# Optimization experiments

Measured on AMD Instinct MI355X. Metric: run time of the kernel, lower is better.

## Reference

```python
import jax, jax.numpy as jnp
import numpy as np

C = 1024
R = 4            # reduction
A = 10           # num_adapters
LN_EPS = 1e-5
THRESHOLDS = np.array([1/9, 1/7, 1/5, 1/3, 1.0, 3.0, 5.0, 7.0, 9.0], dtype=np.float32)


def setup_inputs() -> dict:
    key = jax.random.key(0)
    k_feat, k_ar, k_w1, k_w2 = jax.random.split(key, 4)
    B, NA, H, W = 2, 3, 64, 64
    Cr = C // R
    output_feat = jax.random.normal(k_feat, (B, C, H, W), jnp.float32)
    # aspect ratios in [0,10) so all 10 adapters get selected
    aspect_ratio = jax.random.uniform(k_ar, (B, NA, H, W), jnp.float32) * 10.0
    # LayerNorm params (torch default init: weight=1, bias=0), stacked over adapters
    ln_scale = jnp.ones((A, C), jnp.float32)
    ln_bias = jnp.zeros((A, C), jnp.float32)
    # kaiming_normal_ fan_out / relu: std = sqrt(2/fan_out); torch weight [out,in]
    # w1 here is [C, Cr] == torch weight [Cr, C].T, fan_out = Cr
    w1 = jax.random.normal(k_w1, (A, C, Cr), jnp.float32) * np.sqrt(2.0 / Cr)
    # w2 here is [Cr, C] == torch weight [C, Cr].T, fan_out = C
    w2 = jax.random.normal(k_w2, (A, Cr, C), jnp.float32) * np.sqrt(2.0 / C)
    return dict(output_feat=output_feat, aspect_ratio=aspect_ratio,
                ln_scale=ln_scale, ln_bias=ln_bias, w1=w1, w2=w2)


def reference(output_feat, aspect_ratio, ln_scale, ln_bias, w1, w2):
    B, Cc, H, W = output_feat.shape
    NA = aspect_ratio.shape[1]
    HW = H * W
    # tokens [N, C]
    x = output_feat.transpose(0, 2, 3, 1).reshape(-1, Cc)
    # shared LayerNorm normalization (per-adapter affine applied after)
    mu = jnp.mean(x, axis=-1, keepdims=True)
    var = jnp.var(x, axis=-1, keepdims=True)
    norm = (x - mu) * jax.lax.rsqrt(var + LN_EPS)              # [N, C]
    y = norm[None, :, :] * ln_scale[:, None, :] + ln_bias[:, None, :]  # [A, N, C]
    h = jax.nn.gelu(jnp.einsum('anc,acd->and', y, w1), approximate=False)
    adapter_out = jnp.einsum('and,adc->anc', h, w2)            # [A, N, C]
    adapter_out = adapter_out.reshape(A, B, HW, Cc)            # [A, B, HW, C]
    # per-anchor, per-pixel adapter index from aspect ratio vs thresholds
    thr = jnp.asarray(THRESHOLDS, dtype=aspect_ratio.dtype)
    ar = aspect_ratio.reshape(B, NA, HW)
    idx = jnp.sum(ar[..., None] > thr, axis=-1)                # [B, NA, HW] in [0, 9]
    # gather selected adapter output per (batch, anchor, pixel)
    b_idx = jnp.arange(B)[:, None, None]
    p_idx = jnp.arange(HW)[None, None, :]
    selected = adapter_out[idx, b_idx, p_idx]                  # [B, NA, HW, C]
    selected = selected.mean(axis=1).reshape(B, H, W, Cc).transpose(0, 3, 1, 2)
    return selected + output_feat
```

## Files before the change

### kernel.cpp

```cpp
#include <hip/hip_runtime.h>
#include <hip/hip_bf16.h>
#include <math.h>

#define C_DIM 1024
#define CR    256
#define A_N   10
#define NANCH 3
#define B_N   2
#define HW_N  4096
#define NTOK  (B_N*HW_N)
#define KG2   (A_N*CR)

typedef unsigned short ushort_t;
typedef __attribute__((ext_vector_type(4))) float f32x4;
typedef __attribute__((ext_vector_type(8))) short bf16x8;

__device__ __forceinline__ ushort_t f2bf(float x) {
    __hip_bfloat16 h = __float2bfloat16(x);
    return *reinterpret_cast<ushort_t*>(&h);
}
__device__ __forceinline__ float bf2f(ushort_t u) {
    return __uint_as_float(((unsigned)u) << 16);
}

__device__ __forceinline__ float fast_gelu(float x) {
    float t = x * x;
    float u = x * (-1.5957691216f - 0.0713548163f * t);
    float e = __expf(u);
    return x * __frcp_rn(1.0f + e);
}

__global__ __launch_bounds__(256) void prep_all(
    const float* __restrict__ w1, const float* __restrict__ w2,
    const float* __restrict__ ln_s, const float* __restrict__ ln_b,
    const float* __restrict__ feat, const float* __restrict__ ar,
    ushort_t* __restrict__ w1t, ushort_t* __restrict__ w2t,
    float* __restrict__ bias1, float* __restrict__ sumv, float* __restrict__ sumq,
    int* __restrict__ cnt, int* __restrict__ tokw, int* __restrict__ tokmap) {
    __shared__ float lds[64][65];
    __shared__ float bb[4][64];
    __shared__ int lcnt[A_N], lpos[A_N], gbase[A_N];
    int id = blockIdx.x, tid = threadIdx.x;
    int lo = tid & 63, hi = tid >> 6;

    if (id < 640) {
        int d0 = (id & 3) * 64, c0 = ((id >> 2) & 15) * 64, a = id >> 6;
        #pragma unroll
        for (int i = 0; i < 16; i++) {
            int c_l = i * 4 + hi;
            lds[c_l][lo] = w1[((size_t)a * C_DIM + c0 + c_l) * CR + d0 + lo];
        }
        __syncthreads();
        {
            float s = 0.f;
            #pragma unroll
            for (int cc = 0; cc < 16; cc++) {
                int c = hi * 16 + cc;
                s += lds[c][lo] * ln_b[a * C_DIM + c0 + c];
            }
            bb[hi][lo] = s;
        }
        float sc = ln_s[a * C_DIM + c0 + lo];
        #pragma unroll
        for (int i = 0; i < 16; i++) {
            int d_l = i * 4 + hi;
            w1t[((size_t)a * CR + d0 + d_l) * C_DIM + c0 + lo] = f2bf(lds[lo][d_l] * sc);
        }
        __syncthreads();
        if (hi == 0)
            atomicAdd(&bias1[a * CR + d0 + lo], bb[0][lo] + bb[1][lo] + bb[2][lo] + bb[3][lo]);
    } else if (id < 1280) {
        int id2 = id - 640;
        int k0 = (id2 % 40) * 64, c0 = (id2 / 40) * 64;
        #pragma unroll
        for (int i = 0; i < 16; i++) {
            int k_l = i * 4 + hi;
            lds[k_l][lo] = w2[((size_t)k0 + k_l) * C_DIM + c0 + lo];
        }
        __syncthreads();
        #pragma unroll
        for (int i = 0; i < 16; i++) {
            int c_l = i * 4 + hi;
            w2t[((size_t)c0 + c_l) * KG2 + k0 + lo] = f2bf(lds[lo][c_l]);
        }
    } else if (id < 2304) {
        int id2 = id - 1280;
        int p0 = (id2 & 63) * 64, c0 = ((id2 >> 6) & 7) * 128, b = id2 >> 9;
        int p = lo, cs = hi;
        float s = 0.f, s2 = 0.f;
        #pragma unroll
        for (int c = cs; c < 128; c += 4) {
            float v = feat[((size_t)b * C_DIM + c0 + c) * HW_N + p0 + p];
            s += v; s2 += v * v;
        }
        float (*sh)[64] = (float(*)[64])lds;
        sh[cs][p] = s; sh[cs + 4][p] = s2;
        __syncthreads();
        if (tid < 64) {
            float ss = sh[0][tid] + sh[1][tid] + sh[2][tid] + sh[3][tid];
            float qq = sh[4][tid] + sh[5][tid] + sh[6][tid] + sh[7][tid];
            int t = b * HW_N + p0 + tid;
            atomicAdd(&sumv[t], ss);
            atomicAdd(&sumq[t], qq);
        }
    } else {
        if (tid < A_N) { lcnt[tid] = 0; lpos[tid] = 0; }
        __syncthreads();
        int t = (id - 2304) * 256 + tid;
        int b = t >> 12, p = t & (HW_N - 1);
        const float THR[9] = {1.0f/9.0f, 1.0f/7.0f, 0.2f, 1.0f/3.0f, 1.0f, 3.0f, 5.0f, 7.0f, 9.0f};
        int idxs[NANCH];
        #pragma unroll
        for (int na = 0; na < NANCH; na++) {
            float v = ar[(size_t)b * NANCH * HW_N + na * HW_N + p];
            int idx = 0;
            #pragma unroll
            for (int i = 0; i < 9; i++) idx += (v > THR[i]) ? 1 : 0;
            idxs[na] = idx;
        }
        int myA[NANCH], myC[NANCH], nmine = 0;
        #pragma unroll
        for (int j = 0; j < NANCH; j++) {
            bool first = true; int c3 = 0;
            #pragma unroll
            for (int k = 0; k < NANCH; k++) {
                if (idxs[k] == idxs[j]) { c3++; if (k < j) first = false; }
            }
            if (first) {
                myA[nmine] = idxs[j];
                myC[nmine] = c3;
                nmine++;
                atomicAdd(&lcnt[idxs[j]], 1);
            }
        }
        __syncthreads();
        if (tid < A_N) gbase[tid] = atomicAdd(&cnt[tid], lcnt[tid]);
        __syncthreads();
        for (int i = 0; i < NANCH; i++) {
            if (i < nmine) {
                int a2 = myA[i];
                int slot = atomicAdd(&lpos[a2], 1);
                int pos = gbase[a2] + slot;
                tokw[a2 * NTOK + pos] = t;
                tokmap[t * 3 + i] = pos | (a2 << 13) | (myC[i] << 17);
            } else {
                tokmap[t * 3 + i] = 0;
            }
        }
    }
}

__global__ __launch_bounds__(256) void normk(const float* __restrict__ feat,
                                             const float* __restrict__ sumv,
                                             const float* __restrict__ sumq,
                                             ushort_t* __restrict__ normG) {
    int p0 = blockIdx.x * 64, c0 = blockIdx.y * 64, b = blockIdx.z;
    __shared__ float lds[64][65];
    int tid = threadIdx.x, lo = tid & 63, hi = tid >> 6;
    #pragma unroll
    for (int i = 0; i < 16; i++) {
        int c_l = i * 4 + hi;
        lds[c_l][lo] = feat[((size_t)b * C_DIM + c0 + c_l) * HW_N + p0 + lo];
    }
    __syncthreads();
    #pragma unroll
    for (int i = 0; i < 16; i++) {
        int p_l = i * 4 + hi;
        int t = b * HW_N + p0 + p_l;
        float m = sumv[t] * (1.f / C_DIM);
        float q = sumq[t] * (1.f / C_DIM);
        float r = rsqrtf(q - m * m + 1e-5f);
        normG[(size_t)t * C_DIM + c0 + lo] = f2bf((lds[lo][p_l] - m) * r);
    }
}

__device__ __forceinline__ void gemm_core_ptrs(
    const ushort_t* const ap[4], const ushort_t* const bp[4],
    int K, ushort_t* As, ushort_t* Bs, f32x4 acc[4][4]) {
    const int tid = threadIdx.x;
    const int lane = tid & 63;
    const int w = tid >> 6;
    const int wr = w >> 1, wc = w & 1;
    const int lrow = lane & 15;
    const int quad = lane >> 4;
    const int swzr = lrow & 7;

    #pragma unroll
    for (int i = 0; i < 4; i++)
        #pragma unroll
        for (int j = 0; j < 4; j++)
            #pragma unroll
            for (int e = 0; e < 4; e++) acc[i][j][e] = 0.f;

    for (int k0 = 0; k0 < K; k0 += 64) {
        __syncthreads();
        #pragma unroll
        for (int i = 0; i < 4; i++) {
            __builtin_amdgcn_global_load_lds(
                (__attribute__((address_space(1))) void*)(ap[i] + k0),
                (__attribute__((address_space(3))) void*)(As + (w * 32 + i * 8) * 64),
                16, 0, 0);
            __builtin_amdgcn_global_load_lds(
                (__attribute__((address_space(1))) void*)(bp[i] + k0),
                (__attribute__((address_space(3))) void*)(Bs + (w * 32 + i * 8) * 64),
                16, 0, 0);
        }
        __syncthreads();
        #pragma unroll
        for (int ks = 0; ks < 2; ks++) {
            const int cidx = ((ks * 4 + quad) ^ swzr) * 8;
            bf16x8 af[4], bfr[4];
            #pragma unroll
            for (int mt = 0; mt < 4; mt++)
                af[mt] = *(const bf16x8*)(As + (wr * 64 + mt * 16 + lrow) * 64 + cidx);
            #pragma unroll
            for (int nt = 0; nt < 4; nt++)
                bfr[nt] = *(const bf16x8*)(Bs + (wc * 64 + nt * 16 + lrow) * 64 + cidx);
            #pragma unroll
            for (int mt = 0; mt < 4; mt++)
                #pragma unroll
                for (int nt = 0; nt < 4; nt++)
                    acc[mt][nt] = __builtin_amdgcn_mfma_f32_16x16x32_bf16(af[mt], bfr[nt], acc[mt][nt], 0, 0, 0);
        }
    }
}

__global__ __launch_bounds__(256) void gemm1c(const ushort_t* __restrict__ normG,
                                              const ushort_t* __restrict__ w1t,
                                              const float* __restrict__ bias1,
                                              const int* __restrict__ tokw,
                                              const int* __restrict__ cnt,
                                              ushort_t* __restrict__ Hc) {
    int a = blockIdx.z;
    int mcount = cnt[a];
    int m0 = blockIdx.y * 128;
    if (m0 >= mcount) return;
    int n0 = blockIdx.x * 128;
    int base = 0;
    for (int a2 = 0; a2 < a; a2++) base += cnt[a2];

    __shared__ __align__(16) ushort_t As[128 * 64];
    __shared__ __align__(16) ushort_t Bs[128 * 64];

    int tid = threadIdx.x, lane = tid & 63, w = tid >> 6;
    int lrow8 = lane >> 3;
    int scol = ((lane & 7) ^ lrow8) * 8;
    int srowl = w * 32 + lrow8;

    const ushort_t* ap[4];
    const ushort_t* bp[4];
    #pragma unroll
    for (int i = 0; i < 4; i++) {
        int rt = tokw[a * NTOK + m0 + srowl + i * 8] & (NTOK - 1);
        ap[i] = normG + (size_t)rt * C_DIM + scol;
        bp[i] = w1t + ((size_t)a * CR + n0 + srowl + i * 8) * C_DIM + scol;
    }

    f32x4 acc[4][4];
    gemm_core_ptrs(ap, bp, C_DIM, As, Bs, acc);

    int wr = w >> 1, wc = w & 1, lrow = lane & 15, quad = lane >> 4;
    float bi[4];
    #pragma unroll
    for (int nt = 0; nt < 4; nt++)
        bi[nt] = bias1[a * CR + n0 + wc * 64 + nt * 16 + lrow];
    #pragma unroll
    for (int mt = 0; mt < 4; mt++)
        #pragma unroll
        for (int r = 0; r < 4; r++) {
            int i_row = m0 + wr * 64 + mt * 16 + quad * 4 + r;
            bool live = i_row < mcount;
            #pragma unroll
            for (int nt = 0; nt < 4; nt++) {
                int col = n0 + wc * 64 + nt * 16 + lrow;
                float v = acc[mt][nt][r] + bi[nt];
                if (live)
                    Hc[(size_t)(base + i_row) * CR + col] = f2bf(fast_gelu(v));
            }
        }
}

__global__ __launch_bounds__(256) void gemm2c(const ushort_t* __restrict__ Hc,
                                              const ushort_t* __restrict__ w2t,
                                              const int* __restrict__ cnt,
                                              ushort_t* __restrict__ O) {
    int a = blockIdx.z;
    int mcount = cnt[a];
    int m0 = blockIdx.y * 128;
    if (m0 >= mcount) return;
    int n0 = blockIdx.x * 128;
    int base = 0;
    for (int a2 = 0; a2 < a; a2++) base += cnt[a2];

    __shared__ __align__(16) ushort_t As[128 * 64];
    __shared__ __align__(16) ushort_t Bs[128 * 64];

    int tid = threadIdx.x, lane = tid & 63, w = tid >> 6;
    int lrow8 = lane >> 3;
    int scol = ((lane & 7) ^ lrow8) * 8;
    int srowl = w * 32 + lrow8;

    const ushort_t* ap[4];
    const ushort_t* bp[4];
    #pragma unroll
    for (int i = 0; i < 4; i++) {
        ap[i] = Hc + (size_t)(base + m0 + srowl + i * 8) * CR + scol;
        bp[i] = w2t + (size_t)(n0 + srowl + i * 8) * KG2 + a * CR + scol;
    }

    f32x4 acc[4][4];
    gemm_core_ptrs(ap, bp, CR, As, Bs, acc);

    int wr = w >> 1, wc = w & 1, lrow = lane & 15, quad = lane >> 4;
    #pragma unroll
    for (int mt = 0; mt < 4; mt++)
        #pragma unroll
        for (int r = 0; r < 4; r++) {
            int i_row = m0 + wr * 64 + mt * 16 + quad * 4 + r;
            bool live = i_row < mcount;
            #pragma unroll
            for (int nt = 0; nt < 4; nt++) {
                int col = n0 + wc * 64 + nt * 16 + lrow;
                if (live)
                    O[(size_t)(base + i_row) * C_DIM + col] = f2bf(acc[mt][nt][r]);
            }
        }
}

__global__ __launch_bounds__(256) void finalk2(const ushort_t* __restrict__ O,
                                               const int* __restrict__ tokmap,
                                               const int* __restrict__ cnt,
                                               const float* __restrict__ feat,
                                               float* __restrict__ out) {
    int p0 = blockIdx.x * 64, c0 = blockIdx.y * 64, b = blockIdx.z;
    __shared__ float lds[64][65];
    __shared__ int pbase[A_N];
    int tid = threadIdx.x, lo = tid & 63, hi = tid >> 6;
    if (tid < A_N) {
        int s = 0;
        for (int k = 0; k < tid; k++) s += cnt[k];
        pbase[tid] = s;
    }
    __syncthreads();
    #pragma unroll
    for (int i = 0; i < 16; i++) {
        int tl = i * 4 + hi;
        int t = b * HW_N + p0 + tl;
        float val = 0.f;
        #pragma unroll
        for (int j = 0; j < 3; j++) {
            int e = tokmap[t * 3 + j];
            float wv = (float)(e >> 17) * (1.0f / 3.0f);
            int a2 = (e >> 13) & 15;
            int row = pbase[a2] + (e & 8191);
            val += wv * bf2f(O[(size_t)row * C_DIM + c0 + lo]);
        }
        lds[tl][lo] = val;
    }
    __syncthreads();
    #pragma unroll
    for (int i = 0; i < 16; i++) {
        int c_l = i * 4 + hi;
        size_t o = ((size_t)b * C_DIM + c0 + c_l) * HW_N + p0 + lo;
        out[o] = lds[lo][c_l] + feat[o];
    }
}

extern "C" void kernel_launch(void* const* d_in, const int* in_sizes, int n_in,
                              void* d_out, int out_size, void* d_ws, size_t ws_size,
                              hipStream_t stream) {
    (void)in_sizes; (void)n_in; (void)out_size; (void)ws_size;
    const float* feat = (const float*)d_in[0];
    const float* ar   = (const float*)d_in[1];
    const float* ln_s = (const float*)d_in[2];
    const float* ln_b = (const float*)d_in[3];
    const float* w1   = (const float*)d_in[4];
    const float* w2   = (const float*)d_in[5];
    float* out = (float*)d_out;
    char* ws = (char*)d_ws;

    float*    bias1  = (float*)(ws + 0);
    int*      cnt    = (int*)(ws + 10240);
    float*    sumv   = (float*)(ws + 10496);
    float*    sumq   = (float*)(ws + 43264);
    const size_t ZERO_BYTES = 76800;
    int*      tokmap = (int*)(ws + 76800);
    int*      tokw   = (int*)(ws + 175104);
    ushort_t* w1t    = (ushort_t*)(ws + 502784);
    ushort_t* w2t    = (ushort_t*)(ws + 5745664);
    ushort_t* normG  = (ushort_t*)(ws + 10988544);
    ushort_t* Hc     = (ushort_t*)(ws + 27765760);
    ushort_t* O      = (ushort_t*)(ws + 40414208);

    dim3 blk(256);
    hipMemsetAsync(ws, 0, ZERO_BYTES, stream);
    prep_all<<<dim3(2336), blk, 0, stream>>>(w1, w2, ln_s, ln_b, feat, ar,
                                             w1t, w2t, bias1, sumv, sumq, cnt, tokw, tokmap);
    normk<<<dim3(64, 16, B_N), blk, 0, stream>>>(feat, sumv, sumq, normG);
    gemm1c<<<dim3(2, 64, A_N), blk, 0, stream>>>(normG, w1t, bias1, tokw, cnt, Hc);
    gemm2c<<<dim3(8, 64, A_N), blk, 0, stream>>>(Hc, w2t, cnt, O);
    finalk2<<<dim3(64, 16, B_N), blk, 0, stream>>>(O, tokmap, cnt, feat, out);
}
```

Baseline: 101.4 us.

## Double-buffer LDS tiles in grouped GEMM core to overlap loads with MFMA

Converts the shared GEMM main loop into a two-stage pipeline. The next K-tile is issued into an alternate LDS buffer via global_load_lds while MFMAs run on the current one, with vmcnt waits and explicit barriers. This aims to hide global-load latency that previously stalled between syncthreads. LDS per block doubles to 64KB, which may lower occupancy.

```diff
diff --git a/kernel.cpp b/kernel.cpp
--- a/kernel.cpp
+++ b/kernel.cpp
@@ -192,37 +192,61 @@
             #pragma unroll
             for (int e = 0; e < 4; e++) acc[i][j][e] = 0.f;
 
-    for (int k0 = 0; k0 < K; k0 += 64) {
-        __syncthreads();
-        #pragma unroll
-        for (int i = 0; i < 4; i++) {
-            __builtin_amdgcn_global_load_lds(
-                (__attribute__((address_space(1))) void*)(ap[i] + k0),
-                (__attribute__((address_space(3))) void*)(As + (w * 32 + i * 8) * 64),
-                16, 0, 0);
-            __builtin_amdgcn_global_load_lds(
-                (__attribute__((address_space(1))) void*)(bp[i] + k0),
-                (__attribute__((address_space(3))) void*)(Bs + (w * 32 + i * 8) * 64),
-                16, 0, 0);
-        }
-        __syncthreads();
-        #pragma unroll
-        for (int ks = 0; ks < 2; ks++) {
-            const int cidx = ((ks * 4 + quad) ^ swzr) * 8;
-            bf16x8 af[4], bfr[4];
-            #pragma unroll
-            for (int mt = 0; mt < 4; mt++)
-                af[mt] = *(const bf16x8*)(As + (wr * 64 + mt * 16 + lrow) * 64 + cidx);
-            #pragma unroll
-            for (int nt = 0; nt < 4; nt++)
-                bfr[nt] = *(const bf16x8*)(Bs + (wc * 64 + nt * 16 + lrow) * 64 + cidx);
-            #pragma unroll
-            for (int mt = 0; mt < 4; mt++)
-                #pragma unroll
-                for (int nt = 0; nt < 4; nt++)
-                    acc[mt][nt] = __builtin_amdgcn_mfma_f32_16x16x32_bf16(af[mt], bfr[nt], acc[mt][nt], 0, 0, 0);
-        }
-    }
+#define STAGE(BUF, KOFF)                                                          \
+    do {                                                                          \
+        _Pragma("unroll")                                                         \
+        for (int i = 0; i < 4; i++) {                                             \
+            __builtin_amdgcn_global_load_lds(                                     \
+                (__attribute__((address_space(1))) void*)(ap[i] + (KOFF)),        \
+                (__attribute__((address_space(3))) void*)(As + (BUF) * 8192 + (w * 32 + i * 8) * 64), \
+                16, 0, 0);                                                        \
+            __builtin_amdgcn_global_load_lds(                                     \
+                (__attribute__((address_space(1))) void*)(bp[i] + (KOFF)),        \
+                (__attribute__((address_space(3))) void*)(Bs + (BUF) * 8192 + (w * 32 + i * 8) * 64), \
+                16, 0, 0);                                                        \
+        }                                                                         \
+    } while (0)
+
+#define COMPUTE(BUF)                                                              \
+    do {                                                                          \
+        const ushort_t* Ab = As + (BUF) * 8192;                                   \
+        const ushort_t* Bb = Bs + (BUF) * 8192;                                   \
+        _Pragma("unroll")                                                         \
+        for (int ks = 0; ks < 2; ks++) {                                          \
+            const int cidx = ((ks * 4 + quad) ^ swzr) * 8;                        \
+            bf16x8 af[4], bfr[4];                                                 \
+            _Pragma("unroll")                                                     \
+            for (int mt = 0; mt < 4; mt++)                                        \
+                af[mt] = *(const bf16x8*)(Ab + (wr * 64 + mt * 16 + lrow) * 64 + cidx); \
+            _Pragma("unroll")                                                     \
+            for (int nt = 0; nt < 4; nt++)                                        \
+                bfr[nt] = *(const bf16x8*)(Bb + (wc * 64 + nt * 16 + lrow) * 64 + cidx); \
+            _Pragma("unroll")                                                     \
+            for (int mt = 0; mt < 4; mt++)                                        \
+                _Pragma("unroll")                                                 \
+                for (int nt = 0; nt < 4; nt++)                                    \
+                    acc[mt][nt] = __builtin_amdgcn_mfma_f32_16x16x32_bf16(af[mt], bfr[nt], acc[mt][nt], 0, 0, 0); \
+        }                                                                         \
+    } while (0)
+
+    STAGE(0, 0);
+    int buf = 0;
+    for (int k0 = 64; k0 < K; k0 += 64) {
+        STAGE(buf ^ 1, k0);
+        asm volatile("s_waitcnt vmcnt(8)" ::: "memory");
+        __builtin_amdgcn_s_barrier();
+        __builtin_amdgcn_sched_barrier(0);
+        COMPUTE(buf);
+        __builtin_amdgcn_sched_barrier(0);
+        __builtin_amdgcn_s_barrier();
+        buf ^= 1;
+    }
+    asm volatile("s_waitcnt vmcnt(0)" ::: "memory");
+    __builtin_amdgcn_s_barrier();
+    __builtin_amdgcn_sched_barrier(0);
+    COMPUTE(buf);
+#undef STAGE
+#undef COMPUTE
 }
 
 __global__ __launch_bounds__(256) void gemm1c(const ushort_t* __restrict__ normG,
@@ -239,8 +263,8 @@
     int base = 0;
     for (int a2 = 0; a2 < a; a2++) base += cnt[a2];
 
-    __shared__ __align__(16) ushort_t As[128 * 64];
-    __shared__ __align__(16) ushort_t Bs[128 * 64];
+    __shared__ __align__(16) ushort_t As[2 * 128 * 64];
+    __shared__ __align__(16) ushort_t Bs[2 * 128 * 64];
 
     int tid = threadIdx.x, lane = tid & 63, w = tid >> 6;
     int lrow8 = lane >> 3;
@@ -292,8 +316,8 @@
     int base = 0;
     for (int a2 = 0; a2 < a; a2++) base += cnt[a2];
 
-    __shared__ __align__(16) ushort_t As[128 * 64];
-    __shared__ __align__(16) ushort_t Bs[128 * 64];
+    __shared__ __align__(16) ushort_t As[2 * 128 * 64];
+    __shared__ __align__(16) ushort_t Bs[2 * 128 * 64];
 
     int tid = threadIdx.x, lane = tid & 63, w = tid >> 6;
     int lrow8 = lane >> 3;
```

New measurement: 105.7 us. +4.2%, slower.
